# Performance work log

Hardware: AMD Instinct MI355X
Metric: run time of the kernel (lower is better)

Reference implementation:

```python
import jax, jax.numpy as jnp
import numpy as np

B, F, D, A = 1024, 33, 128, 128  # batch, num_fields, embed_dim, attn_size (A must equal gnn dim)

def setup_inputs() -> dict:
    key = jax.random.key(0)
    k1, k2, k3, k4 = jax.random.split(key, 4)
    gnn_feature = jax.random.normal(k1, (B, A), dtype=jnp.float32)
    x = jax.random.normal(k2, (B, F, D), dtype=jnp.float32)
    # attention Linear(embed_dim -> attn_size): weight (A, D), bias (A,)
    lim = 1.0 / np.sqrt(D)
    attn_W = jax.random.uniform(k3, (A, D), minval=-lim, maxval=lim, dtype=jnp.float32)
    attn_b = jax.random.uniform(k4, (A,), minval=-lim, maxval=lim, dtype=jnp.float32)
    return {"gnn_feature": gnn_feature, "x": x, "attn_W": attn_W, "attn_b": attn_b}

def reference(gnn_feature, x, attn_W, attn_b):
    num_fields = x.shape[1]
    row, col = np.triu_indices(num_fields, k=1)  # P = F*(F-1)/2 pairs
    inner = x[:, row] * x[:, col]                # [B, P, D]
    fm = jax.nn.relu(jnp.einsum('bpd,ad->bpa', inner, attn_W) + attn_b)  # [B, P, A]
    # bmm(gnn[b,1,A], fm[b,p,A,1]) -> dot product per pair, softmax over pairs
    scores = jnp.einsum('ba,bpa->bp', gnn_feature, fm)  # [B, P]
    attn = jax.nn.softmax(scores, axis=1)               # [B, P]
    attn_output = jnp.einsum('bp,bpd->bd', attn, inner) * 100.0  # [B, D]
    return jnp.concatenate([gnn_feature, attn_output], axis=1)   # [B, A+D]
```

## Files before the change

### kernel.cpp

```cpp
#include <hip/hip_runtime.h>

#define FN 33
#define DN 128
#define AN 128
#define PN 528
#define MTN 33
#define XS 136
#define TS 36

typedef __attribute__((ext_vector_type(8))) _Float16 half8;
typedef __attribute__((ext_vector_type(4))) float f32x4;

__device__ __forceinline__ unsigned int pkrtz(float a, float b) {
  return __builtin_bit_cast(unsigned int, __builtin_amdgcn_cvt_pkrtz(a, b));
}

__device__ __forceinline__ float row_sum16(float v) {
  v += __builtin_bit_cast(float, __builtin_amdgcn_update_dpp(0, __builtin_bit_cast(int, v), 0x128, 0xF, 0xF, false));
  v += __builtin_bit_cast(float, __builtin_amdgcn_update_dpp(0, __builtin_bit_cast(int, v), 0x124, 0xF, 0xF, false));
  v += __builtin_bit_cast(float, __builtin_amdgcn_update_dpp(0, __builtin_bit_cast(int, v), 0x122, 0xF, 0xF, false));
  v += __builtin_bit_cast(float, __builtin_amdgcn_update_dpp(0, __builtin_bit_cast(int, v), 0x121, 0xF, 0xF, false));
  return v;
}

__global__ __launch_bounds__(256, 2)
void afm_kernel(const float* __restrict__ gnn, const float* __restrict__ xg,
                const float* __restrict__ Wg,  const float* __restrict__ bg,
                float* __restrict__ out)
{
  __shared__ __align__(16) _Float16 xh[FN * XS];
  __shared__ __align__(16) float attn2d[FN * TS];
  __shared__ __align__(16) float scores_s[PN];
  __shared__ __align__(16) float part[256];
  __shared__ unsigned short rowcol[PN];
  __shared__ float red[8];

  const int tid  = threadIdx.x;
  const int b    = blockIdx.x;
  const int wave = tid >> 6;
  const int lane = tid & 63;
  const int q    = lane >> 4;
  const int u    = lane & 15;

  for (int idx = tid; idx < FN * TS; idx += 256) attn2d[idx] = 0.0f;

  const f32x4* xg4 = (const f32x4*)(xg + (size_t)b * FN * DN);
  for (int idx = tid; idx < (FN * DN) / 4; idx += 256) {
    f32x4 v = xg4[idx];
    int i  = idx >> 5;
    int d0 = (idx & 31) << 2;
    *(uint2*)&xh[i * XS + d0] = make_uint2(pkrtz(v.x, v.y), pkrtz(v.z, v.w));
  }
  for (int p = tid; p < PN; p += 256) {
    int i = 0, rem = p;
    while (rem >= FN - 1 - i) { rem -= FN - 1 - i; i++; }
    rowcol[p] = (unsigned short)(i | ((i + 1 + rem) << 8));
  }

  half8 Bf[8][4];
  #pragma unroll
  for (int n = 0; n < 8; n++) {
    const float* wrow = Wg + (size_t)(n * 16 + u) * DN + q * 8;
    #pragma unroll
    for (int kk = 0; kk < 4; kk++) {
      f32x4 w0 = *(const f32x4*)(wrow + kk * 32);
      f32x4 w1 = *(const f32x4*)(wrow + kk * 32 + 4);
      union { half8 h; unsigned int w[4]; } t;
      t.w[0] = pkrtz(w0.x, w0.y);
      t.w[1] = pkrtz(w0.z, w0.w);
      t.w[2] = pkrtz(w1.x, w1.y);
      t.w[3] = pkrtz(w1.z, w1.w);
      Bf[n][kk] = t.h;
    }
  }
  float garr[8], barr[8];
  #pragma unroll
  for (int n = 0; n < 8; n++) {
    garr[n] = gnn[(size_t)b * AN + n * 16 + u];
    barr[n] = bg[n * 16 + u];
  }
  __syncthreads();

  for (int mt = wave; mt < MTN; mt += 4) {
    const int p = mt * 16 + u;
    const unsigned int rc = rowcol[p];
    const int r = rc & 255, c = rc >> 8;

    half8 Af[4];
    #pragma unroll
    for (int kk = 0; kk < 4; kk++) {
      half8 xr = *(const half8*)&xh[r * XS + kk * 32 + q * 8];
      half8 xc = *(const half8*)&xh[c * XS + kk * 32 + q * 8];
      Af[kk] = xr * xc;
    }

    f32x4 acc[8];
    #pragma unroll
    for (int n = 0; n < 8; n++) acc[n] = (f32x4){0.f, 0.f, 0.f, 0.f};
    #pragma unroll
    for (int kk = 0; kk < 4; kk++)
      #pragma unroll
      for (int n = 0; n < 8; n++)
        acc[n] = __builtin_amdgcn_mfma_f32_16x16x32_f16(Af[kk], Bf[n][kk], acc[n], 0, 0, 0);

    float sc[4] = {0.f, 0.f, 0.f, 0.f};
    #pragma unroll
    for (int n = 0; n < 8; n++)
      #pragma unroll
      for (int rr = 0; rr < 4; rr++) {
        float fmv = acc[n][rr] + barr[n];
        fmv = fmv > 0.f ? fmv : 0.f;
        sc[rr] = fmaf(fmv, garr[n], sc[rr]);
      }
    #pragma unroll
    for (int rr = 0; rr < 4; rr++) sc[rr] = row_sum16(sc[rr]);
    if (u == 0)
      *(f32x4*)&scores_s[mt * 16 + q * 4] = (f32x4){sc[0], sc[1], sc[2], sc[3]};
  }
  __syncthreads();

  float s0 = scores_s[tid];
  float s1 = scores_s[tid + 256];
  float s2 = (tid < 16) ? scores_s[tid + 512] : -3.4e38f;
  float m = fmaxf(fmaxf(s0, s1), s2);
  #pragma unroll
  for (int off = 32; off >= 1; off >>= 1) m = fmaxf(m, __shfl_xor(m, off, 64));
  if (lane == 0) red[wave] = m;
  __syncthreads();
  const float smax = fmaxf(fmaxf(red[0], red[1]), fmaxf(red[2], red[3]));

  float e0 = __expf(s0 - smax);
  float e1 = __expf(s1 - smax);
  float e2 = (tid < 16) ? __expf(s2 - smax) : 0.f;
  {
    unsigned int rc = rowcol[tid];
    attn2d[(rc & 255) * TS + ((rc >> 8) - (rc & 255) - 1)] = e0;
    rc = rowcol[tid + 256];
    attn2d[(rc & 255) * TS + ((rc >> 8) - (rc & 255) - 1)] = e1;
    if (tid < 16) {
      rc = rowcol[tid + 512];
      attn2d[(rc & 255) * TS + ((rc >> 8) - (rc & 255) - 1)] = e2;
    }
  }
  float lsum = e0 + e1 + e2;
  #pragma unroll
  for (int off = 32; off >= 1; off >>= 1) lsum += __shfl_xor(lsum, off, 64);
  if (lane == 0) red[4 + wave] = lsum;
  __syncthreads();
  const float Z = red[4] + red[5] + red[6] + red[7];

  {
    const int d = tid & 127;
    const int h = tid >> 7;
    float xcol[36];
    #pragma unroll
    for (int i = 0; i < FN; i++) xcol[i] = (float)xh[i * XS + d];
    xcol[33] = 0.f; xcol[34] = 0.f; xcol[35] = 0.f;

    float acc = 0.f;
    const int ibeg = h * 16, iend = ibeg + 16;
    #pragma unroll
    for (int i = 0; i < 32; i++) {
      if (i < ibeg || i >= iend) continue;
      const int L = FN - 1 - i;
      const int nf4 = (L + 3) >> 2;
      float ti = 0.f;
      #pragma unroll
      for (int t = 0; t < 8; t++) {
        if (t >= nf4) break;
        f32x4 a4 = *(const f32x4*)&attn2d[i * TS + t * 4];
        ti = fmaf(a4.x, xcol[i + 1 + t * 4 + 0], ti);
        ti = fmaf(a4.y, xcol[i + 1 + t * 4 + 1], ti);
        ti = fmaf(a4.z, xcol[i + 1 + t * 4 + 2], ti);
        ti = fmaf(a4.w, xcol[i + 1 + t * 4 + 3], ti);
      }
      acc = fmaf(xcol[i], ti, acc);
    }
    part[tid] = acc;
  }
  __syncthreads();
  if (tid < DN) {
    float tot = part[tid] + part[tid + 128];
    out[(size_t)b * (AN + DN) + AN + tid] = tot * (100.0f / Z);
  } else {
    const int a = tid - 128;
    out[(size_t)b * (AN + DN) + a] = gnn[(size_t)b * AN + a];
  }
}

extern "C" void kernel_launch(void* const* d_in, const int* in_sizes, int n_in,
                              void* d_out, int out_size, void* d_ws, size_t ws_size,
                              hipStream_t stream) {
  (void)n_in; (void)out_size; (void)d_ws; (void)ws_size;
  const float* gnn  = (const float*)d_in[0];
  const float* x    = (const float*)d_in[1];
  const float* W    = (const float*)d_in[2];
  const float* bias = (const float*)d_in[3];
  float* out = (float*)d_out;
  const int Bn = in_sizes[0] / AN;
  afm_kernel<<<dim3(Bn), dim3(256), 0, stream>>>(gnn, x, W, bias, out);
}
```

Baseline: 116.5 us.

## Process two batch rows per block and pack final weighted sum in fp16x2

Measured after the change: 121.4 us. +4.2%, slower.

```diff
diff --git a/kernel.cpp b/kernel.cpp
--- a/kernel.cpp
+++ b/kernel.cpp
@@ -6,14 +6,18 @@
 #define PN 528
 #define MTN 33
 #define XS 136
-#define TS 36
+#define AS 36
 
 typedef __attribute__((ext_vector_type(8))) _Float16 half8;
+typedef __attribute__((ext_vector_type(2))) _Float16 h2;
 typedef __attribute__((ext_vector_type(4))) float f32x4;
+typedef __attribute__((ext_vector_type(2))) float f32x2;
+typedef __attribute__((ext_vector_type(4))) unsigned int u32x4;
 
 __device__ __forceinline__ unsigned int pkrtz(float a, float b) {
   return __builtin_bit_cast(unsigned int, __builtin_amdgcn_cvt_pkrtz(a, b));
 }
+__device__ __forceinline__ h2 ash2(unsigned int u) { return __builtin_bit_cast(h2, u); }
 
 __device__ __forceinline__ float row_sum16(float v) {
   v += __builtin_bit_cast(float, __builtin_amdgcn_update_dpp(0, __builtin_bit_cast(int, v), 0x128, 0xF, 0xF, false));
@@ -29,34 +33,23 @@
                 float* __restrict__ out)
 {
   __shared__ __align__(16) _Float16 xh[FN * XS];
-  __shared__ __align__(16) float attn2d[FN * TS];
+  __shared__ __align__(16) unsigned int attn_h2[FN * AS];
   __shared__ __align__(16) float scores_s[PN];
-  __shared__ __align__(16) float part[256];
+  __shared__ __align__(16) float part[512];
   __shared__ unsigned short rowcol[PN];
   __shared__ float red[8];
 
   const int tid  = threadIdx.x;
-  const int b    = blockIdx.x;
   const int wave = tid >> 6;
   const int lane = tid & 63;
   const int q    = lane >> 4;
   const int u    = lane & 15;
 
-  for (int idx = tid; idx < FN * TS; idx += 256) attn2d[idx] = 0.0f;
-
-  const f32x4* xg4 = (const f32x4*)(xg + (size_t)b * FN * DN);
-  for (int idx = tid; idx < (FN * DN) / 4; idx += 256) {
-    f32x4 v = xg4[idx];
-    int i  = idx >> 5;
-    int d0 = (idx & 31) << 2;
-    *(uint2*)&xh[i * XS + d0] = make_uint2(pkrtz(v.x, v.y), pkrtz(v.z, v.w));
-  }
   for (int p = tid; p < PN; p += 256) {
     int i = 0, rem = p;
     while (rem >= FN - 1 - i) { rem -= FN - 1 - i; i++; }
     rowcol[p] = (unsigned short)(i | ((i + 1 + rem) << 8));
   }
-
   half8 Bf[8][4];
   #pragma unroll
   for (int n = 0; n < 8; n++) {
@@ -71,120 +64,156 @@
       t.w[2] = pkrtz(w1.x, w1.y);
       t.w[3] = pkrtz(w1.z, w1.w);
       Bf[n][kk] = t.h;
+      asm volatile("" : "+v"(Bf[n][kk]));
     }
   }
-  float garr[8], barr[8];
+  float barr[8];
   #pragma unroll
-  for (int n = 0; n < 8; n++) {
-    garr[n] = gnn[(size_t)b * AN + n * 16 + u];
-    barr[n] = bg[n * 16 + u];
-  }
-  __syncthreads();
-
-  for (int mt = wave; mt < MTN; mt += 4) {
-    const int p = mt * 16 + u;
-    const unsigned int rc = rowcol[p];
-    const int r = rc & 255, c = rc >> 8;
-
-    half8 Af[4];
-    #pragma unroll
-    for (int kk = 0; kk < 4; kk++) {
-      half8 xr = *(const half8*)&xh[r * XS + kk * 32 + q * 8];
-      half8 xc = *(const half8*)&xh[c * XS + kk * 32 + q * 8];
-      Af[kk] = xr * xc;
-    }
-
-    f32x4 acc[8];
-    #pragma unroll
-    for (int n = 0; n < 8; n++) acc[n] = (f32x4){0.f, 0.f, 0.f, 0.f};
-    #pragma unroll
-    for (int kk = 0; kk < 4; kk++)
+  for (int n = 0; n < 8; n++) { barr[n] = bg[n * 16 + u]; asm volatile("" : "+v"(barr[n])); }
+
+  #pragma unroll 1
+  for (int r2 = 0; r2 < 2; r2++) {
+    const int b = blockIdx.x * 2 + r2;
+
+    float garr[8];
+    #pragma unroll
+    for (int n = 0; n < 8; n++) { garr[n] = gnn[(size_t)b * AN + n * 16 + u]; asm volatile("" : "+v"(garr[n])); }
+
+    const f32x4* xg4 = (const f32x4*)(xg + (size_t)b * FN * DN);
+    for (int idx = tid; idx < (FN * DN) / 4; idx += 256) {
+      f32x4 v = xg4[idx];
+      int i  = idx >> 5;
+      int d0 = (idx & 31) << 2;
+      *(uint2*)&xh[i * XS + d0] = make_uint2(pkrtz(v.x, v.y), pkrtz(v.z, v.w));
+    }
+    for (int idx = tid; idx < FN * AS; idx += 256) attn_h2[idx] = 0u;
+    __syncthreads();
+
+    {
+      int mt = wave;
+      unsigned int rc = rowcol[mt * 16 + u];
+      int r = rc & 255, c = rc >> 8;
+      half8 xr[4], xc[4];
       #pragma unroll
-      for (int n = 0; n < 8; n++)
-        acc[n] = __builtin_amdgcn_mfma_f32_16x16x32_f16(Af[kk], Bf[n][kk], acc[n], 0, 0, 0);
-
-    float sc[4] = {0.f, 0.f, 0.f, 0.f};
-    #pragma unroll
-    for (int n = 0; n < 8; n++)
+      for (int kk = 0; kk < 4; kk++) {
+        xr[kk] = *(const half8*)&xh[r * XS + kk * 32 + q * 8];
+        xc[kk] = *(const half8*)&xh[c * XS + kk * 32 + q * 8];
+      }
+      for (;;) {
+        half8 Af[4];
+        #pragma unroll
+        for (int kk = 0; kk < 4; kk++) Af[kk] = xr[kk] * xc[kk];
+
+        const int nmt = mt + 4;
+        if (nmt < MTN) {
+          rc = rowcol[nmt * 16 + u];
+          r = rc & 255; c = rc >> 8;
+          #pragma unroll
+          for (int kk = 0; kk < 4; kk++) {
+            xr[kk] = *(const half8*)&xh[r * XS + kk * 32 + q * 8];
+            xc[kk] = *(const half8*)&xh[c * XS + kk * 32 + q * 8];
+          }
+        }
+
+        float sc[4] = {0.f, 0.f, 0.f, 0.f};
+        #pragma unroll
+        for (int g = 0; g < 2; g++) {
+          f32x4 acc[4];
+          #pragma unroll
+          for (int nn = 0; nn < 4; nn++) {
+            float bv = barr[g * 4 + nn];
+            acc[nn] = (f32x4){bv, bv, bv, bv};
+          }
+          #pragma unroll
+          for (int kk = 0; kk < 4; kk++)
+            #pragma unroll
+            for (int nn = 0; nn < 4; nn++)
+              acc[nn] = __builtin_amdgcn_mfma_f32_16x16x32_f16(Af[kk], Bf[g * 4 + nn][kk], acc[nn], 0, 0, 0);
+          #pragma unroll
+          for (int nn = 0; nn < 4; nn++)
+            #pragma unroll
+            for (int rr = 0; rr < 4; rr++) {
+              float fmv = fmaxf(acc[nn][rr], 0.f);
+              sc[rr] = fmaf(fmv, garr[g * 4 + nn], sc[rr]);
+            }
+        }
+        #pragma unroll
+        for (int rr = 0; rr < 4; rr++) sc[rr] = row_sum16(sc[rr]);
+        if (u == 0)
+          *(f32x4*)&scores_s[mt * 16 + q * 4] = (f32x4){sc[0], sc[1], sc[2], sc[3]};
+
+        if (nmt >= MTN) break;
+        mt = nmt;
+      }
+    }
+    __syncthreads();
+
+    float s0 = scores_s[tid];
+    float s1 = scores_s[tid + 256];
+    float s2 = (tid < 16) ? scores_s[tid + 512] : -3.4e38f;
+    float m = fmaxf(fmaxf(s0, s1), s2);
+    #pragma unroll
+    for (int off = 32; off >= 1; off >>= 1) m = fmaxf(m, __shfl_xor(m, off, 64));
+    if (lane == 0) red[wave] = m;
+    __syncthreads();
+    const float smax = fmaxf(fmaxf(red[0], red[1]), fmaxf(red[2], red[3]));
+
+    float e0 = __expf(s0 - smax);
+    float e1 = __expf(s1 - smax);
+    float e2 = (tid < 16) ? __expf(s2 - smax) : 0.f;
+    {
+      unsigned int rc = rowcol[tid];
+      attn_h2[(rc & 255) * AS + ((rc >> 8) - (rc & 255) - 1)] = pkrtz(e0, e0);
+      rc = rowcol[tid + 256];
+      attn_h2[(rc & 255) * AS + ((rc >> 8) - (rc & 255) - 1)] = pkrtz(e1, e1);
+      if (tid < 16) {
+        rc = rowcol[tid + 512];
+        attn_h2[(rc & 255) * AS + ((rc >> 8) - (rc & 255) - 1)] = pkrtz(e2, e2);
+      }
+    }
+    float lsum = e0 + e1 + e2;
+    #pragma unroll
+    for (int off = 32; off >= 1; off >>= 1) lsum += __shfl_xor(lsum, off, 64);
+    if (lane == 0) red[4 + wave] = lsum;
+    __syncthreads();
+    const float Z = red[4] + red[5] + red[6] + red[7];
+
+    {
+      unsigned int xp[36];
       #pragma unroll
-      for (int rr = 0; rr < 4; rr++) {
-        float fmv = acc[n][rr] + barr[n];
-        fmv = fmv > 0.f ? fmv : 0.f;
-        sc[rr] = fmaf(fmv, garr[n], sc[rr]);
-      }
-    #pragma unroll
-    for (int rr = 0; rr < 4; rr++) sc[rr] = row_sum16(sc[rr]);
-    if (u == 0)
-      *(f32x4*)&scores_s[mt * 16 + q * 4] = (f32x4){sc[0], sc[1], sc[2], sc[3]};
-  }
-  __syncthreads();
-
-  float s0 = scores_s[tid];
-  float s1 = scores_s[tid + 256];
-  float s2 = (tid < 16) ? scores_s[tid + 512] : -3.4e38f;
-  float m = fmaxf(fmaxf(s0, s1), s2);
-  #pragma unroll
-  for (int off = 32; off >= 1; off >>= 1) m = fmaxf(m, __shfl_xor(m, off, 64));
-  if (lane == 0) red[wave] = m;
-  __syncthreads();
-  const float smax = fmaxf(fmaxf(red[0], red[1]), fmaxf(red[2], red[3]));
-
-  float e0 = __expf(s0 - smax);
-  float e1 = __expf(s1 - smax);
-  float e2 = (tid < 16) ? __expf(s2 - smax) : 0.f;
-  {
-    unsigned int rc = rowcol[tid];
-    attn2d[(rc & 255) * TS + ((rc >> 8) - (rc & 255) - 1)] = e0;
-    rc = rowcol[tid + 256];
-    attn2d[(rc & 255) * TS + ((rc >> 8) - (rc & 255) - 1)] = e1;
-    if (tid < 16) {
-      rc = rowcol[tid + 512];
-      attn2d[(rc & 255) * TS + ((rc >> 8) - (rc & 255) - 1)] = e2;
-    }
-  }
-  float lsum = e0 + e1 + e2;
-  #pragma unroll
-  for (int off = 32; off >= 1; off >>= 1) lsum += __shfl_xor(lsum, off, 64);
-  if (lane == 0) red[4 + wave] = lsum;
-  __syncthreads();
-  const float Z = red[4] + red[5] + red[6] + red[7];
-
-  {
-    const int d = tid & 127;
-    const int h = tid >> 7;
-    float xcol[36];
-    #pragma unroll
-    for (int i = 0; i < FN; i++) xcol[i] = (float)xh[i * XS + d];
-    xcol[33] = 0.f; xcol[34] = 0.f; xcol[35] = 0.f;
-
-    float acc = 0.f;
-    const int ibeg = h * 16, iend = ibeg + 16;
-    #pragma unroll
-    for (int i = 0; i < 32; i++) {
-      if (i < ibeg || i >= iend) continue;
-      const int L = FN - 1 - i;
-      const int nf4 = (L + 3) >> 2;
-      float ti = 0.f;
+      for (int j = 0; j < FN; j++) xp[j] = *(const unsigned int*)&xh[j * XS + 2 * lane];
+      xp[33] = 0u; xp[34] = 0u; xp[35] = 0u;
+
+      float a0 = 0.f, a1 = 0.f;
       #pragma unroll
-      for (int t = 0; t < 8; t++) {
-        if (t >= nf4) break;
-        f32x4 a4 = *(const f32x4*)&attn2d[i * TS + t * 4];
-        ti = fmaf(a4.x, xcol[i + 1 + t * 4 + 0], ti);
-        ti = fmaf(a4.y, xcol[i + 1 + t * 4 + 1], ti);
-        ti = fmaf(a4.z, xcol[i + 1 + t * 4 + 2], ti);
-        ti = fmaf(a4.w, xcol[i + 1 + t * 4 + 3], ti);
-      }
-      acc = fmaf(xcol[i], ti, acc);
-    }
-    part[tid] = acc;
-  }
-  __syncthreads();
-  if (tid < DN) {
-    float tot = part[tid] + part[tid + 128];
-    out[(size_t)b * (AN + DN) + AN + tid] = tot * (100.0f / Z);
-  } else {
-    const int a = tid - 128;
-    out[(size_t)b * (AN + DN) + a] = gnn[(size_t)b * AN + a];
+      for (int i = 0; i < 32; i++) {
+        if ((i & 3) != wave) continue;
+        const int L   = 32 - i;
+        const int n4  = (L + 3) >> 2;
+        h2 ti2 = (h2)0.0f;
+        #pragma unroll
+        for (int t = 0; t < 8; t++) {
+          if (t >= n4) break;
+          u32x4 a4 = *(const u32x4*)&attn_h2[i * AS + 4 * t];
+          ti2 += ash2(a4.x) * ash2(xp[i + 1 + 4 * t + 0]);
+          ti2 += ash2(a4.y) * ash2(xp[i + 1 + 4 * t + 1]);
+          ti2 += ash2(a4.z) * ash2(xp[i + 1 + 4 * t + 2]);
+          ti2 += ash2(a4.w) * ash2(xp[i + 1 + 4 * t + 3]);
+        }
+        h2 xi = ash2(xp[i]);
+        a0 = fmaf((float)xi[0], (float)ti2[0], a0);
+        a1 = fmaf((float)xi[1], (float)ti2[1], a1);
+      }
+      *(f32x2*)&part[wave * 128 + 2 * lane] = (f32x2){a0, a1};
+    }
+    __syncthreads();
+    if (tid < DN) {
+      float tot = (part[tid] + part[128 + tid]) + (part[256 + tid] + part[384 + tid]);
+      out[(size_t)b * (AN + DN) + AN + tid] = tot * (100.0f / Z);
+    } else {
+      const int a = tid - 128;
+      out[(size_t)b * (AN + DN) + a] = gnn[(size_t)b * AN + a];
+    }
   }
 }
 
@@ -198,5 +227,5 @@
   const float* bias = (const float*)d_in[3];
   float* out = (float*)d_out;
   const int Bn = in_sizes[0] / AN;
-  afm_kernel<<<dim3(Bn), dim3(256), 0, stream>>>(gnn, x, W, bias, out);
-}
+  afm_kernel<<<dim3(Bn / 2), dim3(256), 0, stream>>>(gnn, x, W, bias, out);
+}
```
